# Performance work log

Hardware: AMD Instinct MI355X
Metric: run time of the kernel (lower is better)

The kernel has to match this reference:

```python
import jax, jax.numpy as jnp
import numpy as np

EPS = 1e-12  # F.normalize eps


def setup_inputs() -> dict:
    key = jax.random.key(0)
    ks = jax.random.split(key, 3)
    B, C, D, R = 4096, 32, 128, 8
    return {
        "source": jax.random.normal(ks[0], (B, C, D), dtype=jnp.float32),
        "data": jax.random.normal(ks[1], (B, C, D), dtype=jnp.float32),
        "W": jax.random.normal(ks[2], (R, D, D), dtype=jnp.float32) * (1.0 / np.sqrt(D)),
        "a": jnp.ones((R, C, D), dtype=jnp.float32),
        "c": jnp.ones((R, C, D), dtype=jnp.float32),
        "d": jnp.zeros((R, C, D), dtype=jnp.float32),
    }


def reference(source, data, W, a, c, d):
    # Generate all reflection directions in one batched GEMM:
    # Linear(bias=False): x @ W_r^T, W_r is [out, in]
    v = jnp.einsum("bci,roi->rbco", source, W)          # [R, B, C, D]
    # DynamicTanh: tanh(a*x)*c + d, params [R, C, D] broadcast over batch
    v = jnp.tanh(a[:, None] * v) * c[:, None] + d[:, None]
    # F.normalize(p=2, dim=-1) with eps clamp
    norm = jnp.linalg.norm(v, axis=-1, keepdims=True)
    v = v / jnp.maximum(norm, EPS)

    # Sequential Householder reflections H_R(...H_2(H_1(x)))
    def step(x, vec):
        dot = jnp.sum(vec * x, axis=-1, keepdims=True)  # [B, C, 1]
        return x - 2.0 * vec * dot, None

    out, _ = jax.lax.scan(step, data, v)
    return out
```

## Files before the change

kernel.cpp:

```cpp
#include <hip/hip_runtime.h>
#include <stdint.h>

#define B_DIM 4096
#define C_DIM 32
#define D_DIM 128
#define R_DIM 8
#define BM    64
#define NTHREADS 256

typedef __bf16 bf16x8 __attribute__((ext_vector_type(8)));
typedef float  f32x4  __attribute__((ext_vector_type(4)));

__device__ __forceinline__ uint32_t f2bf(float f) {
  uint32_t u = __float_as_uint(f);
  return (u + 0x7FFFu + ((u >> 16) & 1u)) >> 16;
}

#if __has_builtin(__builtin_amdgcn_exp2f)
#define EXP2F(x) __builtin_amdgcn_exp2f(x)
#else
#define EXP2F(x) exp2f(x)
#endif
#if __has_builtin(__builtin_amdgcn_rcpf)
#define RCPF(x) __builtin_amdgcn_rcpf(x)
#else
#define RCPF(x) (1.0f / (x))
#endif

__device__ __forceinline__ void load_lds16(const void* g, void* l) {
  __builtin_amdgcn_global_load_lds(
      (const __attribute__((address_space(1))) uint32_t*)g,
      (__attribute__((address_space(3))) uint32_t*)l, 16, 0, 0);
}

template <int CTRL>
__device__ __forceinline__ float ror_add(float v) {
  int r = __builtin_amdgcn_update_dpp(0, __builtin_bit_cast(int, v), CTRL, 0xf, 0xf, true);
  return v + __builtin_bit_cast(float, r);
}
__device__ __forceinline__ float red16(float v) {
  v = ror_add<0x128>(v);
  v = ror_add<0x124>(v);
  v = ror_add<0x122>(v);
  v = ror_add<0x121>(v);
  return v;
}

__global__ void prep_w(const float* __restrict__ W, uint32_t* __restrict__ ws) {
  uint32_t t = blockIdx.x * 256u + threadIdx.x;
  uint32_t c  = t >> 2;
  uint32_t j  = t & 3u;
  uint32_t ln = c & 63u;
  uint32_t kt = (c >> 6) & 3u;
  uint32_t n  = (c >> 8) & 7u;
  uint32_t r  = c >> 11;
  uint32_t o  = n * 16u + (ln & 15u);
  uint32_t k  = kt * 32u + (ln >> 4) * 8u + j * 2u;
  const float2 w2 = *reinterpret_cast<const float2*>(
      W + ((size_t)(r * 128u + o)) * 128u + k);
  ws[t] = f2bf(w2.x) | (f2bf(w2.y) << 16);
}

__global__ void prep_acd(const float* __restrict__ A, const float* __restrict__ C,
                         const float* __restrict__ D, float* __restrict__ oA,
                         uint32_t* __restrict__ oMC) {
  uint32_t t = blockIdx.x * 256u + threadIdx.x;
  uint32_t col = t & 127u, r = (t >> 7) & 7u, c = t >> 10;
  uint32_t in = (r * 32u + c) * 128u + col;
  float av = A[in], cv = C[in], dv = D[in];
  uint32_t idx = (c * 8u + r) * 128u + col;
  oA[idx]  = av * 2.88539008177793f;
  oMC[idx] = (f2bf(cv + dv) << 16) | f2bf(-2.f * cv);
}

__global__ __launch_bounds__(NTHREADS, 4)
void rot_kernel(const float* __restrict__ src, const float* __restrict__ data,
                const uint8_t* __restrict__ wsw, const uint8_t* __restrict__ wsA,
                const uint8_t* __restrict__ wsMC, float* __restrict__ out)
{
  __shared__ __align__(16) unsigned char ldsW[32768];
  __shared__ __align__(16) float    ldsA[8 * 128];
  __shared__ __align__(16) uint32_t ldsMC[8 * 128];

  const uint32_t tid  = threadIdx.x;
  const uint32_t lane = tid & 63u;
  const uint32_t wid  = tid >> 6;
  const uint32_t l15  = lane & 15u;
  const uint32_t lg   = lane >> 4;

  const uint32_t c0   = blockIdx.x & 31u;
  const uint32_t rowb = (blockIdx.x >> 5) * BM + wid * 16u;

  #pragma unroll
  for (int j = 0; j < 8; ++j)
    load_lds16(wsw + wid * 1024u + (uint32_t)j * 4096u + lane * 16u,
               &ldsW[wid * 1024u + (uint32_t)j * 4096u]);
  load_lds16(wsA + (uint32_t)c0 * 4096u + wid * 1024u + lane * 16u,
             (uint8_t*)ldsA + wid * 1024u);
  load_lds16(wsMC + (uint32_t)c0 * 4096u + wid * 1024u + lane * 16u,
             (uint8_t*)ldsMC + wid * 1024u);

  f32x4 x[8];
  #pragma unroll
  for (int q = 0; q < 4; ++q) {
    const float* xr = data + ((size_t)(rowb + lg * 4 + q) * C_DIM + c0) * D_DIM;
    #pragma unroll
    for (int n = 0; n < 8; ++n) x[n][q] = xr[n * 16 + l15];
  }

  bf16x8 af[4];
  {
    const float* sr = src + ((size_t)(rowb + l15) * C_DIM + c0) * D_DIM + lg * 8u;
    #pragma unroll
    for (int kt = 0; kt < 4; ++kt) {
      float4 f0 = *reinterpret_cast<const float4*>(sr + kt * 32);
      float4 f1 = *reinterpret_cast<const float4*>(sr + kt * 32 + 4);
      union { uint32_t u[4]; bf16x8 v; } p;
      p.u[0] = f2bf(f0.x) | (f2bf(f0.y) << 16);
      p.u[1] = f2bf(f0.z) | (f2bf(f0.w) << 16);
      p.u[2] = f2bf(f1.x) | (f2bf(f1.y) << 16);
      p.u[3] = f2bf(f1.z) | (f2bf(f1.w) << 16);
      af[kt] = p.v;
    }
  }

  __syncthreads();

  for (int r = 0; r < R_DIM; ++r) {
    const uint32_t rb = lane * 16u;
    f32x4 acc[8];
    #pragma unroll
    for (int n = 0; n < 8; ++n) acc[n] = (f32x4){0.f, 0.f, 0.f, 0.f};
    #pragma unroll
    for (int kt = 0; kt < 4; ++kt) {
      #pragma unroll
      for (int nh = 0; nh < 8; nh += 4) {
        bf16x8 bq[4];
        #pragma unroll
        for (int i = 0; i < 4; ++i)
          bq[i] = *reinterpret_cast<const bf16x8*>(
              &ldsW[rb + (uint32_t)(((nh + i) * 4 + kt) * 1024)]);
        #pragma unroll
        for (int i = 0; i < 4; ++i)
          acc[nh + i] = __builtin_amdgcn_mfma_f32_16x16x32_bf16(af[kt], bq[i], acc[nh + i], 0, 0, 0);
      }
    }

    __syncthreads();

    if (r < 7) {
      const uint8_t* g = wsw + (uint32_t)(r + 1) * 32768u;
      #pragma unroll
      for (int j = 0; j < 8; ++j)
        load_lds16(g + wid * 1024u + (uint32_t)j * 4096u + lane * 16u,
                   &ldsW[wid * 1024u + (uint32_t)j * 4096u]);
    }

    f32x4 s2 = {0.f,0.f,0.f,0.f}, tx = {0.f,0.f,0.f,0.f};
    #pragma unroll
    for (int n = 0; n < 8; ++n) {
      float    a2  = ldsA [r * 128 + n * 16 + l15];
      uint32_t mcu = ldsMC[r * 128 + n * 16 + l15];
      float m2c = __builtin_bit_cast(float, mcu << 16);
      float cdv = __builtin_bit_cast(float, mcu & 0xffff0000u);
      f32x4 z = acc[n] * a2;
      f32x4 ep;
      #pragma unroll
      for (int q = 0; q < 4; ++q) ep[q] = EXP2F(z[q]);
      ep = ep + 1.0f;
      f32x4 pr;
      #pragma unroll
      for (int q = 0; q < 4; ++q) pr[q] = RCPF(ep[q]);
      f32x4 t = pr * m2c + cdv;
      acc[n] = t;
      s2 = s2 + t * t;
      tx = tx + t * x[n];
    }
    f32x4 sc;
    #pragma unroll
    for (int q = 0; q < 4; ++q) {
      float s = red16(s2[q]);
      float d = red16(tx[q]);
      sc[q] = -2.f * d * RCPF(fmaxf(s, 1e-24f));
    }
    #pragma unroll
    for (int n = 0; n < 8; ++n)
      x[n] = x[n] + sc * acc[n];

    __syncthreads();
  }

  #pragma unroll
  for (int q = 0; q < 4; ++q) {
    float* orow = out + ((size_t)(rowb + lg * 4 + q) * C_DIM + c0) * D_DIM;
    #pragma unroll
    for (int n = 0; n < 8; ++n) orow[n * 16 + l15] = x[n][q];
  }
}

extern "C" void kernel_launch(void* const* d_in, const int* in_sizes, int n_in,
                              void* d_out, int out_size, void* d_ws, size_t ws_size,
                              hipStream_t stream) {
  const float* src  = (const float*)d_in[0];
  const float* data = (const float*)d_in[1];
  const float* W    = (const float*)d_in[2];
  const float* Aa   = (const float*)d_in[3];
  const float* Cc   = (const float*)d_in[4];
  const float* Dd   = (const float*)d_in[5];
  float* out = (float*)d_out;

  uint8_t* wsW  = (uint8_t*)d_ws;
  uint8_t* wsA  = wsW + 262144;
  uint8_t* wsMC = wsA + 131072;

  prep_w<<<dim3(256), dim3(256), 0, stream>>>(W, (uint32_t*)wsW);
  prep_acd<<<dim3(128), dim3(256), 0, stream>>>(Aa, Cc, Dd, (float*)wsA, (uint32_t*)wsMC);

  dim3 grid((B_DIM / BM) * C_DIM);
  dim3 block(NTHREADS);
  rot_kernel<<<grid, block, 0, stream>>>(src, data, wsW, wsA, wsMC, out);
}
```

Baseline: 82.85 us.

## Split W staging into halves and overlap epilogue with second-half MFMAs

```diff
diff --git a/kernel.cpp b/kernel.cpp
--- a/kernel.cpp
+++ b/kernel.cpp
@@ -47,13 +47,14 @@
 }
 
 __global__ void prep_w(const float* __restrict__ W, uint32_t* __restrict__ ws) {
-  uint32_t t = blockIdx.x * 256u + threadIdx.x;
-  uint32_t c  = t >> 2;
+  uint32_t t  = blockIdx.x * 256u + threadIdx.x;
   uint32_t j  = t & 3u;
-  uint32_t ln = c & 63u;
-  uint32_t kt = (c >> 6) & 3u;
-  uint32_t n  = (c >> 8) & 7u;
-  uint32_t r  = c >> 11;
+  uint32_t ln = (t >> 2) & 63u;
+  uint32_t kt = (t >> 8) & 3u;
+  uint32_t nl = (t >> 10) & 3u;
+  uint32_t nh = (t >> 12) & 1u;
+  uint32_t r  = (t >> 13) & 7u;
+  uint32_t n  = nh * 4u + nl;
   uint32_t o  = n * 16u + (ln & 15u);
   uint32_t k  = kt * 32u + (ln >> 4) * 8u + j * 2u;
   const float2 w2 = *reinterpret_cast<const float2*>(
@@ -73,6 +74,96 @@
   oMC[idx] = (f2bf(cv + dv) << 16) | f2bf(-2.f * cv);
 }
 
+__device__ __forceinline__ void stage_half(const uint8_t* __restrict__ wsw,
+                                           unsigned char* ldsW, uint32_t r1,
+                                           uint32_t nh, uint32_t wid, uint32_t lane) {
+  const uint8_t* g = wsw + (r1 * 2u + nh) * 16384u;
+  unsigned char* d = ldsW + nh * 16384u;
+  #pragma unroll
+  for (int j = 0; j < 4; ++j)
+    load_lds16(g + wid * 1024u + (uint32_t)j * 4096u + lane * 16u,
+               d + wid * 1024u + (uint32_t)j * 4096u);
+}
+
+__device__ __forceinline__ void epi_one(int r, int n, const float* ldsA,
+                                        const uint32_t* ldsMC, uint32_t l15,
+                                        f32x4& accn, const f32x4& xn,
+                                        f32x4& s2, f32x4& tx) {
+  float    a2  = ldsA [r * 128 + n * 16 + l15];
+  uint32_t mcu = ldsMC[r * 128 + n * 16 + l15];
+  float m2c = __builtin_bit_cast(float, mcu << 16);
+  float cdv = __builtin_bit_cast(float, mcu & 0xffff0000u);
+  f32x4 z = accn * a2;
+  f32x4 ep;
+  #pragma unroll
+  for (int q = 0; q < 4; ++q) ep[q] = EXP2F(z[q]);
+  ep = ep + 1.0f;
+  f32x4 pr;
+  #pragma unroll
+  for (int q = 0; q < 4; ++q) pr[q] = RCPF(ep[q]);
+  f32x4 t = pr * m2c + cdv;
+  accn = t;
+  s2 = s2 + t * t;
+  tx = tx + t * xn;
+}
+
+template <int R>
+__device__ __forceinline__ void iter_body(
+    const uint8_t* __restrict__ wsw, unsigned char* ldsW,
+    const float* ldsA, const uint32_t* ldsMC,
+    uint32_t lane, uint32_t wid, uint32_t l15,
+    const bf16x8 (&af)[4], f32x4 (&x)[8])
+{
+  f32x4 acc[8];
+  #pragma unroll
+  for (int n = 0; n < 8; ++n) acc[n] = (f32x4){0.f, 0.f, 0.f, 0.f};
+
+  #pragma unroll
+  for (int kt = 0; kt < 4; ++kt) {
+    bf16x8 bq[4];
+    #pragma unroll
+    for (int nl = 0; nl < 4; ++nl)
+      bq[nl] = *reinterpret_cast<const bf16x8*>(
+          &ldsW[(uint32_t)((nl * 4 + kt) * 1024) + lane * 16u]);
+    #pragma unroll
+    for (int nl = 0; nl < 4; ++nl)
+      acc[nl] = __builtin_amdgcn_mfma_f32_16x16x32_bf16(af[kt], bq[nl], acc[nl], 0, 0, 0);
+  }
+
+  __syncthreads();
+  if constexpr (R < 7) stage_half(wsw, ldsW, R + 1, 0, wid, lane);
+
+  f32x4 s2 = {0.f,0.f,0.f,0.f}, tx = {0.f,0.f,0.f,0.f};
+  #pragma unroll
+  for (int kt = 0; kt < 4; ++kt) {
+    bf16x8 bq[4];
+    #pragma unroll
+    for (int nl = 0; nl < 4; ++nl)
+      bq[nl] = *reinterpret_cast<const bf16x8*>(
+          &ldsW[16384u + (uint32_t)((nl * 4 + kt) * 1024) + lane * 16u]);
+    #pragma unroll
+    for (int nl = 0; nl < 4; ++nl)
+      acc[4 + nl] = __builtin_amdgcn_mfma_f32_16x16x32_bf16(af[kt], bq[nl], acc[4 + nl], 0, 0, 0);
+    epi_one(R, kt, ldsA, ldsMC, l15, acc[kt], x[kt], s2, tx);
+  }
+  #pragma unroll
+  for (int n = 4; n < 8; ++n)
+    epi_one(R, n, ldsA, ldsMC, l15, acc[n], x[n], s2, tx);
+  f32x4 sc;
+  #pragma unroll
+  for (int q = 0; q < 4; ++q) {
+    float s = red16(s2[q]);
+    float d = red16(tx[q]);
+    sc[q] = -2.f * d * RCPF(fmaxf(s, 1e-24f));
+  }
+  #pragma unroll
+  for (int n = 0; n < 8; ++n)
+    x[n] = x[n] + sc * acc[n];
+
+  __syncthreads();
+  if constexpr (R < 7) stage_half(wsw, ldsW, R + 1, 1, wid, lane);
+}
+
 __global__ __launch_bounds__(NTHREADS, 4)
 void rot_kernel(const float* __restrict__ src, const float* __restrict__ data,
                 const uint8_t* __restrict__ wsw, const uint8_t* __restrict__ wsA,
@@ -91,10 +182,8 @@
   const uint32_t c0   = blockIdx.x & 31u;
   const uint32_t rowb = (blockIdx.x >> 5) * BM + wid * 16u;
 
-  #pragma unroll
-  for (int j = 0; j < 8; ++j)
-    load_lds16(wsw + wid * 1024u + (uint32_t)j * 4096u + lane * 16u,
-               &ldsW[wid * 1024u + (uint32_t)j * 4096u]);
+  stage_half(wsw, ldsW, 0, 0, wid, lane);
+  stage_half(wsw, ldsW, 0, 1, wid, lane);
   load_lds16(wsA + (uint32_t)c0 * 4096u + wid * 1024u + lane * 16u,
              (uint8_t*)ldsA + wid * 1024u);
   load_lds16(wsMC + (uint32_t)c0 * 4096u + wid * 1024u + lane * 16u,
@@ -126,69 +215,14 @@
 
   __syncthreads();
 
-  for (int r = 0; r < R_DIM; ++r) {
-    const uint32_t rb = lane * 16u;
-    f32x4 acc[8];
-    #pragma unroll
-    for (int n = 0; n < 8; ++n) acc[n] = (f32x4){0.f, 0.f, 0.f, 0.f};
-    #pragma unroll
-    for (int kt = 0; kt < 4; ++kt) {
-      #pragma unroll
-      for (int nh = 0; nh < 8; nh += 4) {
-        bf16x8 bq[4];
-        #pragma unroll
-        for (int i = 0; i < 4; ++i)
-          bq[i] = *reinterpret_cast<const bf16x8*>(
-              &ldsW[rb + (uint32_t)(((nh + i) * 4 + kt) * 1024)]);
-        #pragma unroll
-        for (int i = 0; i < 4; ++i)
-          acc[nh + i] = __builtin_amdgcn_mfma_f32_16x16x32_bf16(af[kt], bq[i], acc[nh + i], 0, 0, 0);
-      }
-    }
-
-    __syncthreads();
-
-    if (r < 7) {
-      const uint8_t* g = wsw + (uint32_t)(r + 1) * 32768u;
-      #pragma unroll
-      for (int j = 0; j < 8; ++j)
-        load_lds16(g + wid * 1024u + (uint32_t)j * 4096u + lane * 16u,
-                   &ldsW[wid * 1024u + (uint32_t)j * 4096u]);
-    }
-
-    f32x4 s2 = {0.f,0.f,0.f,0.f}, tx = {0.f,0.f,0.f,0.f};
-    #pragma unroll
-    for (int n = 0; n < 8; ++n) {
-      float    a2  = ldsA [r * 128 + n * 16 + l15];
-      uint32_t mcu = ldsMC[r * 128 + n * 16 + l15];
-      float m2c = __builtin_bit_cast(float, mcu << 16);
-      float cdv = __builtin_bit_cast(float, mcu & 0xffff0000u);
-      f32x4 z = acc[n] * a2;
-      f32x4 ep;
-      #pragma unroll
-      for (int q = 0; q < 4; ++q) ep[q] = EXP2F(z[q]);
-      ep = ep + 1.0f;
-      f32x4 pr;
-      #pragma unroll
-      for (int q = 0; q < 4; ++q) pr[q] = RCPF(ep[q]);
-      f32x4 t = pr * m2c + cdv;
-      acc[n] = t;
-      s2 = s2 + t * t;
-      tx = tx + t * x[n];
-    }
-    f32x4 sc;
-    #pragma unroll
-    for (int q = 0; q < 4; ++q) {
-      float s = red16(s2[q]);
-      float d = red16(tx[q]);
-      sc[q] = -2.f * d * RCPF(fmaxf(s, 1e-24f));
-    }
-    #pragma unroll
-    for (int n = 0; n < 8; ++n)
-      x[n] = x[n] + sc * acc[n];
-
-    __syncthreads();
-  }
+  iter_body<0>(wsw, ldsW, ldsA, ldsMC, lane, wid, l15, af, x);
+  iter_body<1>(wsw, ldsW, ldsA, ldsMC, lane, wid, l15, af, x);
+  iter_body<2>(wsw, ldsW, ldsA, ldsMC, lane, wid, l15, af, x);
+  iter_body<3>(wsw, ldsW, ldsA, ldsMC, lane, wid, l15, af, x);
+  iter_body<4>(wsw, ldsW, ldsA, ldsMC, lane, wid, l15, af, x);
+  iter_body<5>(wsw, ldsW, ldsA, ldsMC, lane, wid, l15, af, x);
+  iter_body<6>(wsw, ldsW, ldsA, ldsMC, lane, wid, l15, af, x);
+  iter_body<7>(wsw, ldsW, ldsA, ldsMC, lane, wid, l15, af, x);
 
   #pragma unroll
   for (int q = 0; q < 4; ++q) {
```

Result: slower. 88.06 us (+6.3%).

## Load W and activation params directly from global memory, dropping LDS staging

Applied to the files above, without the earlier changes.

```diff
diff --git a/kernel.cpp b/kernel.cpp
--- a/kernel.cpp
+++ b/kernel.cpp
@@ -26,12 +26,6 @@
 #else
 #define RCPF(x) (1.0f / (x))
 #endif
-
-__device__ __forceinline__ void load_lds16(const void* g, void* l) {
-  __builtin_amdgcn_global_load_lds(
-      (const __attribute__((address_space(1))) uint32_t*)g,
-      (__attribute__((address_space(3))) uint32_t*)l, 16, 0, 0);
-}
 
 template <int CTRL>
 __device__ __forceinline__ float ror_add(float v) {
@@ -75,13 +69,9 @@
 
 __global__ __launch_bounds__(NTHREADS, 4)
 void rot_kernel(const float* __restrict__ src, const float* __restrict__ data,
-                const uint8_t* __restrict__ wsw, const uint8_t* __restrict__ wsA,
-                const uint8_t* __restrict__ wsMC, float* __restrict__ out)
+                const uint8_t* __restrict__ wsw, const float* __restrict__ wsA,
+                const uint32_t* __restrict__ wsMC, float* __restrict__ out)
 {
-  __shared__ __align__(16) unsigned char ldsW[32768];
-  __shared__ __align__(16) float    ldsA[8 * 128];
-  __shared__ __align__(16) uint32_t ldsMC[8 * 128];
-
   const uint32_t tid  = threadIdx.x;
   const uint32_t lane = tid & 63u;
   const uint32_t wid  = tid >> 6;
@@ -90,15 +80,6 @@
 
   const uint32_t c0   = blockIdx.x & 31u;
   const uint32_t rowb = (blockIdx.x >> 5) * BM + wid * 16u;
-
-  #pragma unroll
-  for (int j = 0; j < 8; ++j)
-    load_lds16(wsw + wid * 1024u + (uint32_t)j * 4096u + lane * 16u,
-               &ldsW[wid * 1024u + (uint32_t)j * 4096u]);
-  load_lds16(wsA + (uint32_t)c0 * 4096u + wid * 1024u + lane * 16u,
-             (uint8_t*)ldsA + wid * 1024u);
-  load_lds16(wsMC + (uint32_t)c0 * 4096u + wid * 1024u + lane * 16u,
-             (uint8_t*)ldsMC + wid * 1024u);
 
   f32x4 x[8];
   #pragma unroll
@@ -124,43 +105,30 @@
     }
   }
 
-  __syncthreads();
-
   for (int r = 0; r < R_DIM; ++r) {
-    const uint32_t rb = lane * 16u;
+    const bf16x8* wb = reinterpret_cast<const bf16x8*>(
+        wsw + (uint32_t)r * 32768u + lane * 16u);
     f32x4 acc[8];
     #pragma unroll
     for (int n = 0; n < 8; ++n) acc[n] = (f32x4){0.f, 0.f, 0.f, 0.f};
     #pragma unroll
     for (int kt = 0; kt < 4; ++kt) {
+      bf16x8 bq[8];
       #pragma unroll
-      for (int nh = 0; nh < 8; nh += 4) {
-        bf16x8 bq[4];
-        #pragma unroll
-        for (int i = 0; i < 4; ++i)
-          bq[i] = *reinterpret_cast<const bf16x8*>(
-              &ldsW[rb + (uint32_t)(((nh + i) * 4 + kt) * 1024)]);
-        #pragma unroll
-        for (int i = 0; i < 4; ++i)
-          acc[nh + i] = __builtin_amdgcn_mfma_f32_16x16x32_bf16(af[kt], bq[i], acc[nh + i], 0, 0, 0);
-      }
+      for (int n = 0; n < 8; ++n)
+        bq[n] = wb[(uint32_t)(n * 4 + kt) * 64u];
+      #pragma unroll
+      for (int n = 0; n < 8; ++n)
+        acc[n] = __builtin_amdgcn_mfma_f32_16x16x32_bf16(af[kt], bq[n], acc[n], 0, 0, 0);
     }
 
-    __syncthreads();
-
-    if (r < 7) {
-      const uint8_t* g = wsw + (uint32_t)(r + 1) * 32768u;
-      #pragma unroll
-      for (int j = 0; j < 8; ++j)
-        load_lds16(g + wid * 1024u + (uint32_t)j * 4096u + lane * 16u,
-                   &ldsW[wid * 1024u + (uint32_t)j * 4096u]);
-    }
-
+    const float*    pA = wsA  + (uint32_t)(c0 * 8 + r) * 128u;
+    const uint32_t* pM = wsMC + (uint32_t)(c0 * 8 + r) * 128u;
     f32x4 s2 = {0.f,0.f,0.f,0.f}, tx = {0.f,0.f,0.f,0.f};
     #pragma unroll
     for (int n = 0; n < 8; ++n) {
-      float    a2  = ldsA [r * 128 + n * 16 + l15];
-      uint32_t mcu = ldsMC[r * 128 + n * 16 + l15];
+      float    a2  = pA[n * 16 + l15];
+      uint32_t mcu = pM[n * 16 + l15];
       float m2c = __builtin_bit_cast(float, mcu << 16);
       float cdv = __builtin_bit_cast(float, mcu & 0xffff0000u);
       f32x4 z = acc[n] * a2;
@@ -186,8 +154,6 @@
     #pragma unroll
     for (int n = 0; n < 8; ++n)
       x[n] = x[n] + sc * acc[n];
-
-    __syncthreads();
   }
 
   #pragma unroll
@@ -218,5 +184,6 @@
 
   dim3 grid((B_DIM / BM) * C_DIM);
   dim3 block(NTHREADS);
-  rot_kernel<<<grid, block, 0, stream>>>(src, data, wsW, wsA, wsMC, out);
+  rot_kernel<<<grid, block, 0, stream>>>(src, data, wsW, (const float*)wsA,
+                                         (const uint32_t*)wsMC, out);
 }
```

Measured after the change: 135.5 us. 1.64x slower.

## Interleave per-column MFMA with tanh epilogue and pack a/c/d params

Applied to the files above, without the earlier changes.

```diff
diff --git a/kernel.cpp b/kernel.cpp
--- a/kernel.cpp
+++ b/kernel.cpp
@@ -62,25 +62,24 @@
 }
 
 __global__ void prep_acd(const float* __restrict__ A, const float* __restrict__ C,
-                         const float* __restrict__ D, float* __restrict__ oA,
-                         uint32_t* __restrict__ oMC) {
+                         const float* __restrict__ D, uint2* __restrict__ o) {
   uint32_t t = blockIdx.x * 256u + threadIdx.x;
   uint32_t col = t & 127u, r = (t >> 7) & 7u, c = t >> 10;
   uint32_t in = (r * 32u + c) * 128u + col;
   float av = A[in], cv = C[in], dv = D[in];
-  uint32_t idx = (c * 8u + r) * 128u + col;
-  oA[idx]  = av * 2.88539008177793f;
-  oMC[idx] = (f2bf(cv + dv) << 16) | f2bf(-2.f * cv);
+  uint2 v;
+  v.x = __float_as_uint(av * 2.88539008177793f);
+  v.y = (f2bf(cv + dv) << 16) | f2bf(-2.f * cv);
+  o[(c * 8u + r) * 128u + col] = v;
 }
 
 __global__ __launch_bounds__(NTHREADS, 4)
 void rot_kernel(const float* __restrict__ src, const float* __restrict__ data,
-                const uint8_t* __restrict__ wsw, const uint8_t* __restrict__ wsA,
-                const uint8_t* __restrict__ wsMC, float* __restrict__ out)
+                const uint8_t* __restrict__ wsw, const uint8_t* __restrict__ wsACD,
+                float* __restrict__ out)
 {
   __shared__ __align__(16) unsigned char ldsW[32768];
-  __shared__ __align__(16) float    ldsA[8 * 128];
-  __shared__ __align__(16) uint32_t ldsMC[8 * 128];
+  __shared__ __align__(16) uint2 ldsACD[8 * 128];
 
   const uint32_t tid  = threadIdx.x;
   const uint32_t lane = tid & 63u;
@@ -95,10 +94,10 @@
   for (int j = 0; j < 8; ++j)
     load_lds16(wsw + wid * 1024u + (uint32_t)j * 4096u + lane * 16u,
                &ldsW[wid * 1024u + (uint32_t)j * 4096u]);
-  load_lds16(wsA + (uint32_t)c0 * 4096u + wid * 1024u + lane * 16u,
-             (uint8_t*)ldsA + wid * 1024u);
-  load_lds16(wsMC + (uint32_t)c0 * 4096u + wid * 1024u + lane * 16u,
-             (uint8_t*)ldsMC + wid * 1024u);
+  #pragma unroll
+  for (int j = 0; j < 2; ++j)
+    load_lds16(wsACD + (uint32_t)c0 * 8192u + wid * 1024u + (uint32_t)j * 4096u + lane * 16u,
+               (uint8_t*)ldsACD + wid * 1024u + (uint32_t)j * 4096u);
 
   f32x4 x[8];
   #pragma unroll
@@ -128,21 +127,41 @@
 
   for (int r = 0; r < R_DIM; ++r) {
     const uint32_t rb = lane * 16u;
+    const uint2* acd = ldsACD + r * 128;
     f32x4 acc[8];
-    #pragma unroll
-    for (int n = 0; n < 8; ++n) acc[n] = (f32x4){0.f, 0.f, 0.f, 0.f};
-    #pragma unroll
-    for (int kt = 0; kt < 4; ++kt) {
-      #pragma unroll
-      for (int nh = 0; nh < 8; nh += 4) {
-        bf16x8 bq[4];
+    f32x4 s2 = {0.f,0.f,0.f,0.f}, tx = {0.f,0.f,0.f,0.f};
+
+    #pragma unroll
+    for (int n = 0; n < 8; ++n) {
+      bf16x8 bq[4];
+      #pragma unroll
+      for (int kt = 0; kt < 4; ++kt)
+        bq[kt] = *reinterpret_cast<const bf16x8*>(
+            &ldsW[rb + (uint32_t)((n * 4 + kt) * 1024)]);
+      f32x4 a = (f32x4){0.f, 0.f, 0.f, 0.f};
+      #pragma unroll
+      for (int kt = 0; kt < 4; ++kt)
+        a = __builtin_amdgcn_mfma_f32_16x16x32_bf16(af[kt], bq[kt], a, 0, 0, 0);
+      acc[n] = a;
+
+      if (n >= 4) {
+        const int m = n - 4;
+        uint2 w = acd[m * 16 + l15];
+        float a2  = __builtin_bit_cast(float, w.x);
+        float m2c = __builtin_bit_cast(float, w.y << 16);
+        float cdv = __builtin_bit_cast(float, w.y & 0xffff0000u);
+        f32x4 z = acc[m] * a2;
+        f32x4 ep;
         #pragma unroll
-        for (int i = 0; i < 4; ++i)
-          bq[i] = *reinterpret_cast<const bf16x8*>(
-              &ldsW[rb + (uint32_t)(((nh + i) * 4 + kt) * 1024)]);
+        for (int q = 0; q < 4; ++q) ep[q] = EXP2F(z[q]);
+        ep = ep + 1.0f;
+        f32x4 pr;
         #pragma unroll
-        for (int i = 0; i < 4; ++i)
-          acc[nh + i] = __builtin_amdgcn_mfma_f32_16x16x32_bf16(af[kt], bq[i], acc[nh + i], 0, 0, 0);
+        for (int q = 0; q < 4; ++q) pr[q] = RCPF(ep[q]);
+        f32x4 t = pr * m2c + cdv;
+        acc[m] = t;
+        s2 = s2 + t * t;
+        tx = tx + t * x[m];
       }
     }
 
@@ -156,13 +175,12 @@
                    &ldsW[wid * 1024u + (uint32_t)j * 4096u]);
     }
 
-    f32x4 s2 = {0.f,0.f,0.f,0.f}, tx = {0.f,0.f,0.f,0.f};
-    #pragma unroll
-    for (int n = 0; n < 8; ++n) {
-      float    a2  = ldsA [r * 128 + n * 16 + l15];
-      uint32_t mcu = ldsMC[r * 128 + n * 16 + l15];
-      float m2c = __builtin_bit_cast(float, mcu << 16);
-      float cdv = __builtin_bit_cast(float, mcu & 0xffff0000u);
+    #pragma unroll
+    for (int n = 4; n < 8; ++n) {
+      uint2 w = acd[n * 16 + l15];
+      float a2  = __builtin_bit_cast(float, w.x);
+      float m2c = __builtin_bit_cast(float, w.y << 16);
+      float cdv = __builtin_bit_cast(float, w.y & 0xffff0000u);
       f32x4 z = acc[n] * a2;
       f32x4 ep;
       #pragma unroll
@@ -209,14 +227,13 @@
   const float* Dd   = (const float*)d_in[5];
   float* out = (float*)d_out;
 
-  uint8_t* wsW  = (uint8_t*)d_ws;
-  uint8_t* wsA  = wsW + 262144;
-  uint8_t* wsMC = wsA + 131072;
+  uint8_t* wsW   = (uint8_t*)d_ws;
+  uint8_t* wsACD = wsW + 262144;
 
   prep_w<<<dim3(256), dim3(256), 0, stream>>>(W, (uint32_t*)wsW);
-  prep_acd<<<dim3(128), dim3(256), 0, stream>>>(Aa, Cc, Dd, (float*)wsA, (uint32_t*)wsMC);
+  prep_acd<<<dim3(128), dim3(256), 0, stream>>>(Aa, Cc, Dd, (uint2*)wsACD);
 
   dim3 grid((B_DIM / BM) * C_DIM);
   dim3 block(NTHREADS);
-  rot_kernel<<<grid, block, 0, stream>>>(src, data, wsW, wsA, wsMC, out);
-}
+  rot_kernel<<<grid, block, 0, stream>>>(src, data, wsW, wsACD, out);
+}
```

New measurement: 85.49 us. +3.2%, slower.
